# Optimization experiments

Measured on AMD Instinct MI355X. Metric: run time of the kernel, lower is better.

Reference implementation:

```python
import jax, jax.numpy as jnp
import numpy as np
from jax import lax

B, T, C = 2, 1024, 2048
H, N = 32, 64
LAYER_ID, N_LAYER = 1, 24
EPS = 1e-5 * 64.0  # 1e-5 * head_size_divisor**2, divisor=8
RESCALE_T = 256.0 * 0.7  # bf16_limit * 0.7


def setup_inputs():
    key = jax.random.key(0)
    ks = jax.random.split(key, 16)
    r01 = LAYER_ID / (N_LAYER - 1)
    r10 = 1.0 - LAYER_ID / N_LAYER
    ddd = np.arange(C, dtype=np.float64) / C
    pw = lambda p: jnp.asarray(1.0 - ddd ** p, jnp.float32)
    n = np.arange(C, dtype=np.float64)
    decay = -7.0 + 5.0 * (n / (C - 1)) ** (0.85 + r01 ** 0.5)
    sc = lambda k, shp, s: jax.random.normal(k, shp, jnp.float32) * s
    return {
        'x': sc(ks[0], (B, T, C), 1.0),
        'v_first': sc(ks[1], (B, T, C), 1.0),
        'x_r': pw(0.2 * r10), 'x_w': pw(0.9 * r10),
        'x_k': jnp.asarray(1.0 - (ddd ** (0.9 * r10) + 0.4 * r01), jnp.float32),
        'x_v': jnp.asarray(1.0 - (ddd ** (0.4 * r10) + 0.6 * r01), jnp.float32),
        'x_a': pw(0.9 * r10), 'x_g': pw(0.2 * r10),
        'w0': jnp.asarray(decay + 0.5, jnp.float32),
        'w1': sc(ks[2], (C, 64), 0.02), 'w2': sc(ks[3], (64, C), 0.02),
        'a0': jnp.zeros((C,), jnp.float32),
        'a1': sc(ks[4], (C, 64), 0.02), 'a2': sc(ks[5], (64, C), 0.02),
        'v0': jnp.ones((C,), jnp.float32),
        'v1': sc(ks[6], (C, 32), 0.02), 'v2': sc(ks[7], (32, C), 0.02),
        'g1': sc(ks[8], (C, 128), 0.02), 'g2': sc(ks[9], (128, C), 0.02),
        'k_k': jnp.full((C,), 0.85, jnp.float32),
        'k_a': jnp.ones((C,), jnp.float32),
        'r_k': sc(ks[10], (H, N), 0.05),
        'W_r': sc(ks[11], (C, C), C ** -0.5),
        'W_k': sc(ks[12], (C, C), C ** -0.5),
        'W_v': sc(ks[13], (C, C), C ** -0.5),
        'W_o': sc(ks[14], (C, C), C ** -0.5),
        'ln_w': jnp.ones((C,), jnp.float32),
        'ln_b': jnp.zeros((C,), jnp.float32),
    }


def wkv7(r, w, k, v, a, b):
    # RWKV-7 per-head linear state recurrence: S <- S*diag(w) + S a b^T + v k^T; out = S r
    Bsz, Tlen, Cd = r.shape
    to = lambda t: t.reshape(Bsz, Tlen, H, N).transpose(1, 0, 2, 3)  # (T,B,H,N)
    rr, kk, vv, aa, bb = map(to, (r, k, v, a, b))
    ww = jnp.exp(-jnp.exp(to(w)))  # decay in (0,1); w <= -0.5 guaranteed upstream

    def step(S, xs):
        rt, wt, kt, vt, at, bt = xs
        sa = jnp.einsum('bhij,bhj->bhi', S, at)
        S = S * wt[:, :, None, :] + sa[..., None] * bt[:, :, None, :] + vt[..., None] * kt[:, :, None, :]
        return S, jnp.einsum('bhij,bhj->bhi', S, rt)

    S0 = jnp.zeros((Bsz, H, N, N), r.dtype)
    _, out = lax.scan(step, S0, (rr, ww, kk, vv, aa, bb))
    return out.transpose(1, 0, 2, 3).reshape(Bsz, Tlen, Cd)


def reference(x, v_first, x_r, x_w, x_k, x_v, x_a, x_g, w0, w1, w2, a0, a1, a2,
              v0, v1, v2, g1, g2, k_k, k_a, r_k, W_r, W_k, W_v, W_o, ln_w, ln_b):
    # token shift (ZeroPad2d((0,0,1,-1)))
    xx = jnp.concatenate([jnp.zeros_like(x[:, :1]), x[:, :-1]], axis=1) - x
    xr = x + xx * x_r; xw = x + xx * x_w; xk = x + xx * x_k
    xv = x + xx * x_v; xa = x + xx * x_a; xg = x + xx * x_g
    r = xr @ W_r.T
    w = -jax.nn.softplus(-(w0 + jnp.tanh(xw @ w1) @ w2)) - 0.5  # soft clamp to (-inf,-0.5]
    k = xk @ W_k.T
    v = xv @ W_v.T
    # layer_id > 0: value residual gated toward v_first (with max-abs rescales)
    v1p = xv @ v1
    v1p = v1p / jnp.maximum(jnp.max(jnp.abs(v1p)), 1.0)
    v2p = v1p @ v2
    v2p = v2p / jnp.maximum(jnp.max(jnp.abs(v2p)), 1.0)
    gate = jax.nn.sigmoid(jnp.clip(v0 + v2p, -16.0, 16.0))
    vd = v_first - v
    vd = vd / jnp.maximum(jnp.max(jnp.abs(vd)), 1.0)
    v = v + vd * gate
    a = jax.nn.sigmoid(a0 + (xa @ a1) @ a2)
    g = jax.nn.sigmoid(xg @ g1) @ g2
    kk = (k * k_k).reshape(B, T, H, N)
    kk = (kk / jnp.maximum(jnp.linalg.norm(kk, axis=-1, keepdims=True), 1e-12)).reshape(B, T, C)
    k = k * (1.0 + (a - 1.0) * k_a)
    y = wkv7(r, w, k, v, -kk, kk * a)
    needs_rescale = jnp.max(jnp.abs(y)) > RESCALE_T
    # GroupNorm: H groups of size N
    yg = y.reshape(B, T, H, N)
    mu = yg.mean(-1, keepdims=True)
    var = yg.var(-1, keepdims=True)
    y = ((yg - mu) / jnp.sqrt(var + EPS)).reshape(B, T, C) * ln_w + ln_b
    y = y + ((r.reshape(B, T, H, N) * k.reshape(B, T, H, N) * r_k).sum(-1, keepdims=True)
             * v.reshape(B, T, H, N)).reshape(B, T, C)
    y = (y * g) @ W_o.T
    y = jnp.where(needs_rescale, y * 0.5, y)
    v_first_out = jnp.where(needs_rescale, v_first * 0.5, v_first)
    return y, v_first_out
```

## Files before the change

### kernel.cpp

```cpp
#include <hip/hip_runtime.h>
#include <hip/hip_bf16.h>

#define ELq 4194304
#define Cq 2048
#define Tq 1024
#define Hq 32
#define Mq 2048

typedef __attribute__((ext_vector_type(8))) short bf16x8;
typedef __attribute__((ext_vector_type(4))) float f32x4;

__device__ __forceinline__ unsigned short f2bu(float f) {
  union { float f; unsigned u; } v; v.f = f;
  unsigned r = v.u + 0x7fffu + ((v.u >> 16) & 1u);
  return (unsigned short)(r >> 16);
}
__device__ __forceinline__ float b2f(unsigned short u) {
  union { unsigned u; float f; } v; v.u = ((unsigned)u) << 16;
  return v.f;
}
__device__ __forceinline__ void gl_lds16(const void* g, void* l) {
  __builtin_amdgcn_global_load_lds((const __attribute__((address_space(1))) unsigned int*)g,
                                   (__attribute__((address_space(3))) unsigned int*)l, 16, 0, 0);
}

template<int CTRL>
__device__ __forceinline__ float dpp_add(float x) {
  int t = __builtin_amdgcn_update_dpp(0, __builtin_bit_cast(int, x), CTRL, 0xF, 0xF, true);
  return x + __builtin_bit_cast(float, t);
}

struct ConvJob { const float* src; unsigned short* dst; int rows, cols, trans; };
struct ConvJobs { ConvJob j[12]; };

__global__ void k_conv(ConvJobs jobs) {
  ConvJob jb = jobs.j[blockIdx.z];
  int n = jb.rows * jb.cols;
  if (!jb.trans) {
    int n4 = n >> 2;
    for (int i = blockIdx.x * blockDim.x + threadIdx.x; i < n4; i += gridDim.x * blockDim.x) {
      float4 v = ((const float4*)jb.src)[i];
      ushort4 o;
      o.x = f2bu(v.x); o.y = f2bu(v.y); o.z = f2bu(v.z); o.w = f2bu(v.w);
      ((ushort4*)jb.dst)[i] = o;
    }
  } else {
    for (int i = blockIdx.x * blockDim.x + threadIdx.x; i < n; i += gridDim.x * blockDim.x) {
      int col = i / jb.rows;
      int row = i - col * jb.rows;
      jb.dst[i] = f2bu(jb.src[(size_t)row * jb.cols + col]);
    }
  }
}

__global__ void k_zero(unsigned int* p) { if (threadIdx.x < 8) p[threadIdx.x] = 0u; }

__global__ void k_prologue(const float* __restrict__ x,
    const float* __restrict__ mr, const float* __restrict__ mw, const float* __restrict__ mk,
    const float* __restrict__ mv, const float* __restrict__ ma, const float* __restrict__ mg,
    unsigned short* __restrict__ xr, unsigned short* __restrict__ xw, unsigned short* __restrict__ xk,
    unsigned short* __restrict__ xv, unsigned short* __restrict__ xa, unsigned short* __restrict__ xg)
{
  int i4 = blockIdx.x * 256 + threadIdx.x;
  if (i4 >= ELq / 4) return;
  int i = i4 << 2;
  float4 xc = *(const float4*)(x + i);
  int t = (i >> 11) & (Tq - 1);
  float4 xp = make_float4(0.f, 0.f, 0.f, 0.f);
  if (t) xp = *(const float4*)(x + i - Cq);
  float4 dx = make_float4(xp.x - xc.x, xp.y - xc.y, xp.z - xc.z, xp.w - xc.w);
  int c = i & (Cq - 1);
  auto mix = [&](const float* __restrict__ m, unsigned short* __restrict__ o) {
    float4 mm = *(const float4*)(m + c);
    ushort4 u;
    u.x = f2bu(xc.x + dx.x * mm.x); u.y = f2bu(xc.y + dx.y * mm.y);
    u.z = f2bu(xc.z + dx.z * mm.z); u.w = f2bu(xc.w + dx.w * mm.w);
    *(ushort4*)(o + i) = u;
  };
  mix(mr, xr); mix(mw, xw); mix(mk, xk); mix(mv, xv); mix(ma, xa); mix(mg, xg);
}

struct GJob {
  const unsigned short* A; const unsigned short* B;
  const float* bias; float* Cf; unsigned short* Cb;
  unsigned int* amax; const float* aux;
  int K; int ld; int epi;
  float* kkp; float* abp; const float* kkw; const float* kaw;
};
struct GJobs { GJob j[4]; };

__device__ __forceinline__ void epi_store(int epi, float v, size_t o,
    float* Cf, unsigned short* Cb, const float* bias, const float* aux, int col, float& lmax)
{
  switch (epi) {
    case 0: Cf[o] = v; break;
    case 1: Cf[o] = v + bias[col]; break;
    case 2: Cf[o] = 1.f / (1.f + expf(-(v + bias[col]))); break;
    case 4: Cb[o] = f2bu(v); break;
    case 7: lmax = fmaxf(lmax, fabsf(v)); Cf[o] = v; break;
    case 9: lmax = fmaxf(lmax, fabsf(aux[o] - v)); Cf[o] = v; break;
    case 10: {
      float wv = v + bias[col];
      float wlog = -log1pf(expf(-wv)) - 0.5f;
      Cf[o] = expf(-expf(wlog));
      break;
    }
  }
}

__global__ __launch_bounds__(256, 2) void k_gemm128(GJobs jobs) {
  GJob jb = jobs.j[blockIdx.z];
  __shared__ __align__(16) unsigned short As[128 * 32];
  __shared__ __align__(16) unsigned short Bs[128 * 32];
  __shared__ float sred[4];
  const int tid = threadIdx.x, lane = tid & 63, wid = tid >> 6;
  const int wr = wid >> 1, wc = wid & 1;
  const int lin = blockIdx.y * 16 + blockIdx.x;
  const int swz = (lin & 7) * 32 + (lin >> 3);
  const int m0 = (swz >> 4) * 128, n0 = (swz & 15) * 128;
  const int K = jb.K, ld = jb.ld;
  const unsigned short* A = jb.A; const unsigned short* B = jb.B;
  f32x4 acc[4][4] = {};
  for (int k0 = 0; k0 < K; k0 += 32) {
    #pragma unroll
    for (int i = 0; i < 2; ++i) {
      int cw = wid * 64 + i * 256;
      int c = cw + lane;
      int row = c >> 2, q = c & 3;
      gl_lds16(A + (size_t)(m0 + row) * ld + k0 + q * 8, &As[cw * 8]);
      gl_lds16(B + (size_t)(n0 + row) * ld + k0 + q * 8, &Bs[cw * 8]);
    }
    __syncthreads();
    const int kg = (lane >> 4) * 8;
    bf16x8 af[4], bq[4];
    #pragma unroll
    for (int mi = 0; mi < 4; ++mi)
      af[mi] = *(const bf16x8*)&As[(wr * 64 + mi * 16 + (lane & 15)) * 32 + kg];
    #pragma unroll
    for (int ni = 0; ni < 4; ++ni)
      bq[ni] = *(const bf16x8*)&Bs[(wc * 64 + ni * 16 + (lane & 15)) * 32 + kg];
    #pragma unroll
    for (int mi = 0; mi < 4; ++mi)
      #pragma unroll
      for (int ni = 0; ni < 4; ++ni)
        acc[mi][ni] = __builtin_amdgcn_mfma_f32_16x16x32_bf16(af[mi], bq[ni], acc[mi][ni], 0, 0, 0);
    __syncthreads();
  }
  if (jb.epi == 11) {
    float kkwv[4], kawv[4]; int colv[4];
    #pragma unroll
    for (int ni = 0; ni < 4; ++ni) {
      colv[ni] = n0 + wc * 64 + ni * 16 + (lane & 15);
      kkwv[ni] = jb.kkw[colv[ni]];
      kawv[ni] = jb.kaw[colv[ni]];
    }
    #pragma unroll
    for (int mi = 0; mi < 4; ++mi) {
      #pragma unroll
      for (int q = 0; q < 4; ++q) {
        float kkv[4]; float ss = 0.f;
        #pragma unroll
        for (int ni = 0; ni < 4; ++ni) {
          kkv[ni] = acc[mi][ni][q] * kkwv[ni];
          ss += kkv[ni] * kkv[ni];
        }
        ss = dpp_add<0xB1>(ss); ss = dpp_add<0x4E>(ss);
        ss = dpp_add<0x141>(ss); ss = dpp_add<0x140>(ss);
        float inv = 1.f / fmaxf(sqrtf(ss), 1e-12f);
        int row = m0 + wr * 64 + mi * 16 + ((lane >> 4) << 2) + q;
        #pragma unroll
        for (int ni = 0; ni < 4; ++ni) {
          size_t o = (size_t)row * 2048 + colv[ni];
          float kraw = acc[mi][ni][q];
          float kkn = kkv[ni] * inv;
          float as = jb.abp[o];
          jb.kkp[o] = -kkn;
          jb.abp[o] = kkn * as;
          jb.Cf[o] = kraw * (1.f + (as - 1.f) * kawv[ni]);
        }
      }
    }
    return;
  }
  float lmax = 0.f;
  #pragma unroll
  for (int mi = 0; mi < 4; ++mi)
    #pragma unroll
    for (int ni = 0; ni < 4; ++ni) {
      int col = n0 + wc * 64 + ni * 16 + (lane & 15);
      int row = m0 + wr * 64 + mi * 16 + ((lane >> 4) << 2);
      #pragma unroll
      for (int q = 0; q < 4; ++q)
        epi_store(jb.epi, acc[mi][ni][q], (size_t)(row + q) * 2048 + col,
                  jb.Cf, jb.Cb, jb.bias, jb.aux, col, lmax);
    }
  if (jb.epi == 7 || jb.epi == 9) {
    #pragma unroll
    for (int o = 32; o; o >>= 1) lmax = fmaxf(lmax, __shfl_xor(lmax, o));
    if (lane == 0) sred[wid] = lmax;
    __syncthreads();
    if (tid == 0)
      atomicMax(jb.amax, __float_as_uint(fmaxf(fmaxf(sred[0], sred[1]), fmaxf(sred[2], sred[3]))));
  }
}

template<int TBN>
__global__ __launch_bounds__(256, 2) void k_gemmN_sk(GJob jb) {
  __shared__ __align__(16) unsigned short As[128 * 32];
  __shared__ __align__(16) unsigned short Bs[TBN * 32];
  const int tid = threadIdx.x, lane = tid & 63, wid = tid >> 6;
  const int m0 = blockIdx.x * 128;
  const int koff = blockIdx.y * 256;
  const int ld = jb.ld;
  constexpr int NF = TBN / 16;
  const unsigned short* A = jb.A + koff;
  const unsigned short* B = jb.B + koff;
  float* out = jb.Cf + (size_t)blockIdx.y * (2048 * TBN);
  f32x4 acc[2][NF] = {};
  for (int k0 = 0; k0 < 256; k0 += 32) {
    for (int cw = wid * 64; cw < 512; cw += 256) {
      int c = cw + lane; int row = c >> 2, q = c & 3;
      gl_lds16(A + (size_t)(m0 + row) * ld + k0 + q * 8, &As[cw * 8]);
    }
    for (int cw = wid * 64; cw < TBN * 4; cw += 256) {
      int c = cw + lane; int row = c >> 2, q = c & 3;
      gl_lds16(B + (size_t)row * ld + k0 + q * 8, &Bs[cw * 8]);
    }
    __syncthreads();
    const int kg = (lane >> 4) * 8;
    bf16x8 af[2], bq[NF];
    #pragma unroll
    for (int mi = 0; mi < 2; ++mi)
      af[mi] = *(const bf16x8*)&As[(wid * 32 + mi * 16 + (lane & 15)) * 32 + kg];
    #pragma unroll
    for (int ni = 0; ni < NF; ++ni)
      bq[ni] = *(const bf16x8*)&Bs[(ni * 16 + (lane & 15)) * 32 + kg];
    #pragma unroll
    for (int mi = 0; mi < 2; ++mi)
      #pragma unroll
      for (int ni = 0; ni < NF; ++ni)
        acc[mi][ni] = __builtin_amdgcn_mfma_f32_16x16x32_bf16(af[mi], bq[ni], acc[mi][ni], 0, 0, 0);
    __syncthreads();
  }
  #pragma unroll
  for (int mi = 0; mi < 2; ++mi)
    #pragma unroll
    for (int ni = 0; ni < NF; ++ni) {
      int col = ni * 16 + (lane & 15);
      int row = m0 + wid * 32 + mi * 16 + ((lane >> 4) << 2);
      #pragma unroll
      for (int q = 0; q < 4; ++q)
        out[(size_t)(row + q) * TBN + col] = acc[mi][ni][q];
    }
}

__global__ void k_skepi(const float* __restrict__ pw, const float* __restrict__ pa,
                        const float* __restrict__ pv, const float* __restrict__ pg,
                        unsigned short* __restrict__ hw, unsigned short* __restrict__ ha,
                        unsigned short* __restrict__ hv, unsigned short* __restrict__ hg,
                        unsigned int* __restrict__ amax) {
  int i = blockIdx.x * 256 + threadIdx.x;
  const float* src; unsigned short* dst; int stride, mode, loc;
  if (i < 131072)      { src = pw; dst = hw; stride = 131072; mode = 0; loc = i; }
  else if (i < 262144) { src = pa; dst = ha; stride = 131072; mode = 1; loc = i - 131072; }
  else if (i < 327680) { src = pv; dst = hv; stride = 65536;  mode = 2; loc = i - 262144; }
  else                 { src = pg; dst = hg; stride = 262144; mode = 3; loc = i - 327680; }
  float s = 0.f;
  #pragma unroll
  for (int sp = 0; sp < 8; ++sp) s += src[loc + (size_t)sp * stride];
  float lmax = 0.f, o;
  switch (mode) {
    case 0: o = tanhf(s); break;
    case 1: o = s; break;
    case 2: o = s; lmax = fabsf(s); break;
    default: o = 1.f / (1.f + expf(-s)); break;
  }
  dst[loc] = f2bu(o);
  #pragma unroll
  for (int of = 32; of; of >>= 1) lmax = fmaxf(lmax, __shfl_xor(lmax, of));
  if ((threadIdx.x & 63) == 0 && lmax > 0.f) atomicMax(amax, __float_as_uint(lmax));
}

__global__ void k_vfin(float* __restrict__ v, const float* __restrict__ vf,
                       const float* __restrict__ z, const float* __restrict__ v0c,
                       const unsigned int* __restrict__ sc) {
  int i4 = blockIdx.x * 256 + threadIdx.x;
  if (i4 >= ELq / 4) return;
  int i = i4 << 2;
  float m1 = fmaxf(__uint_as_float(sc[0]), 1.f);
  float m2 = fmaxf(__uint_as_float(sc[1]) / m1, 1.f);
  float inv12 = 1.f / (m1 * m2);
  float invvd = 1.f / fmaxf(__uint_as_float(sc[2]), 1.f);
  int c = i & (Cq - 1);
  float4 zv = *(const float4*)(z + i);
  float4 vv = *(const float4*)(v + i);
  float4 fv = *(const float4*)(vf + i);
  float4 v0v = *(const float4*)(v0c + c);
  float4 o;
  #pragma unroll
  for (int j = 0; j < 4; ++j) {
    float gx = (&v0v.x)[j] + (&zv.x)[j] * inv12;
    gx = fminf(fmaxf(gx, -16.f), 16.f);
    float gate = 1.f / (1.f + expf(-gx));
    float vr = (&vv.x)[j];
    (&o.x)[j] = vr + ((&fv.x)[j] - vr) * (gate * invvd);
  }
  *(float4*)(v + i) = o;
}

struct SRg { float4 r, w, k, a, b; float v; };

__device__ __forceinline__ void ld_g(SRg& R,
    const float* __restrict__ rS, const float* __restrict__ wS, const float* __restrict__ kS,
    const float* __restrict__ vS, const float* __restrict__ aS, const float* __restrict__ bS,
    size_t sb, int cl, int row) {
  R.r = *(const float4*)(rS + sb + cl);
  R.w = *(const float4*)(wS + sb + cl);
  R.k = *(const float4*)(kS + sb + cl);
  R.a = *(const float4*)(aS + sb + cl);
  R.b = *(const float4*)(bS + sb + cl);
  R.v = vS[sb + row];
}

__device__ __forceinline__ void wkv_step(const SRg& R, float S[4], float& ymx,
    float* __restrict__ y, size_t yoff, int lane) {
  float sa = (S[0]*R.a.x + S[1]*R.a.y) + (S[2]*R.a.z + S[3]*R.a.w);
  sa = dpp_add<0xB1>(sa);
  sa = dpp_add<0x4E>(sa);
  sa = dpp_add<0x141>(sa);
  sa = dpp_add<0x140>(sa);
  float vi = R.v;
  float s0 = S[0]*R.w.x + (sa*R.b.x + vi*R.k.x);
  float s1 = S[1]*R.w.y + (sa*R.b.y + vi*R.k.y);
  float s2 = S[2]*R.w.z + (sa*R.b.z + vi*R.k.z);
  float s3 = S[3]*R.w.w + (sa*R.b.w + vi*R.k.w);
  S[0]=s0; S[1]=s1; S[2]=s2; S[3]=s3;
  float yp = (s0*R.r.x + s1*R.r.y) + (s2*R.r.z + s3*R.r.w);
  yp = dpp_add<0xB1>(yp);
  yp = dpp_add<0x4E>(yp);
  yp = dpp_add<0x141>(yp);
  yp = dpp_add<0x140>(yp);
  if ((lane & 15) == 0) {
    y[yoff] = yp;
    ymx = fmaxf(ymx, fabsf(yp));
  }
}

__global__ __launch_bounds__(64, 1) void k_wkv(
    const float* __restrict__ rS, const float* __restrict__ wS, const float* __restrict__ kS,
    const float* __restrict__ vS, const float* __restrict__ aS, const float* __restrict__ bS,
    float* __restrict__ y, unsigned int* __restrict__ ymax) {
  const int lane = threadIdx.x;
  const int bh = blockIdx.x & 63;
  const int rq = blockIdx.x >> 6;
  const int row = rq * 4 + (lane >> 4);
  const int cl = (lane & 15) * 4;
  float S[4];
  #pragma unroll
  for (int q = 0; q < 4; ++q) S[q] = 0.f;
  const size_t base0 = (size_t)(bh >> 5) * Tq * Cq + (size_t)(bh & 31) * 64;

  SRg R0, R1, R2, R3;
  ld_g(R0, rS, wS, kS, vS, aS, bS, base0,          cl, row);
  ld_g(R1, rS, wS, kS, vS, aS, bS, base0 + Cq,     cl, row);
  ld_g(R2, rS, wS, kS, vS, aS, bS, base0 + 2 * Cq, cl, row);
  ld_g(R3, rS, wS, kS, vS, aS, bS, base0 + 3 * Cq, cl, row);

  float ymx = 0.f;
  for (int t = 0; t < Tq; t += 4) {
    int t4 = (t + 4 < Tq) ? t + 4 : Tq - 1;
    int t5 = (t + 5 < Tq) ? t + 5 : Tq - 1;
    int t6 = (t + 6 < Tq) ? t + 6 : Tq - 1;
    int t7 = (t + 7 < Tq) ? t + 7 : Tq - 1;
    wkv_step(R0, S, ymx, y, base0 + (size_t)t * Cq + row, lane);
    ld_g(R0, rS, wS, kS, vS, aS, bS, base0 + (size_t)t4 * Cq, cl, row);
    wkv_step(R1, S, ymx, y, base0 + (size_t)(t + 1) * Cq + row, lane);
    ld_g(R1, rS, wS, kS, vS, aS, bS, base0 + (size_t)t5 * Cq, cl, row);
    wkv_step(R2, S, ymx, y, base0 + (size_t)(t + 2) * Cq + row, lane);
    ld_g(R2, rS, wS, kS, vS, aS, bS, base0 + (size_t)t6 * Cq, cl, row);
    wkv_step(R3, S, ymx, y, base0 + (size_t)(t + 3) * Cq + row, lane);
    ld_g(R3, rS, wS, kS, vS, aS, bS, base0 + (size_t)t7 * Cq, cl, row);
  }
  #pragma unroll
  for (int o = 32; o; o >>= 1) ymx = fmaxf(ymx, __shfl_xor(ymx, o));
  if (lane == 0) atomicMax(ymax, __float_as_uint(ymx));
}

__global__ __launch_bounds__(256) void k_epi1(const float* __restrict__ y, const float* __restrict__ r,
    const float* __restrict__ k, const float* __restrict__ v, const unsigned short* __restrict__ g,
    const float* __restrict__ lnw, const float* __restrict__ lnb, const float* __restrict__ rk,
    unsigned short* __restrict__ yg) {
  int wid = threadIdx.x >> 6, lane = threadIdx.x & 63;
  int idx = blockIdx.x * 4 + wid;
  size_t off = (size_t)idx * 64 + lane;
  int c = ((idx & (Hq - 1)) << 6) | lane;
  float yv = y[off];
  float s = yv;
  #pragma unroll
  for (int o = 32; o; o >>= 1) s += __shfl_xor(s, o);
  float mu = s * (1.f / 64.f);
  float d = yv - mu;
  float vs = d * d;
  #pragma unroll
  for (int o = 32; o; o >>= 1) vs += __shfl_xor(vs, o);
  float yn = d / sqrtf(vs * (1.f / 64.f) + 6.4e-4f);
  float yo = yn * lnw[c] + lnb[c];
  float bon = r[off] * k[off] * rk[c];
  #pragma unroll
  for (int o = 32; o; o >>= 1) bon += __shfl_xor(bon, o);
  yo += bon * v[off];
  yg[off] = f2bu(yo * b2f(g[off]));
}

__global__ void k_wo_fin(const float* __restrict__ p0, const float* __restrict__ p1,
                         const unsigned int* __restrict__ sc, float* __restrict__ out) {
  int i = blockIdx.x * 256 + threadIdx.x;
  if (i >= ELq / 4) return;
  float s = (__uint_as_float(sc[3]) > 179.2f) ? 0.5f : 1.f;
  float4 a = ((const float4*)p0)[i];
  float4 b = ((const float4*)p1)[i];
  ((float4*)out)[i] = make_float4((a.x + b.x) * s, (a.y + b.y) * s,
                                  (a.z + b.z) * s, (a.w + b.w) * s);
}

__global__ void k_vout(const float* __restrict__ vf, const unsigned int* __restrict__ sc,
                       float* __restrict__ out) {
  int i = blockIdx.x * 256 + threadIdx.x;
  if (i >= ELq) return;
  float s = (__uint_as_float(sc[3]) > 179.2f) ? 0.5f : 1.f;
  out[i] = vf[i] * s;
}

extern "C" void kernel_launch(void* const* d_in, const int* in_sizes, int n_in,
                              void* d_out, int out_size, void* d_ws, size_t ws_size,
                              hipStream_t stream) {
  const float* x      = (const float*)d_in[0];
  const float* vfirst = (const float*)d_in[1];
  const float* x_r = (const float*)d_in[2];
  const float* x_w = (const float*)d_in[3];
  const float* x_k = (const float*)d_in[4];
  const float* x_v = (const float*)d_in[5];
  const float* x_a = (const float*)d_in[6];
  const float* x_g = (const float*)d_in[7];
  const float* w0 = (const float*)d_in[8];
  const float* w1 = (const float*)d_in[9];
  const float* w2 = (const float*)d_in[10];
  const float* a0 = (const float*)d_in[11];
  const float* a1 = (const float*)d_in[12];
  const float* a2 = (const float*)d_in[13];
  const float* v0 = (const float*)d_in[14];
  const float* v1 = (const float*)d_in[15];
  const float* v2 = (const float*)d_in[16];
  const float* g1 = (const float*)d_in[17];
  const float* g2 = (const float*)d_in[18];
  const float* k_k = (const float*)d_in[19];
  const float* k_a = (const float*)d_in[20];
  const float* r_k = (const float*)d_in[21];
  const float* W_r = (const float*)d_in[22];
  const float* W_k = (const float*)d_in[23];
  const float* W_v = (const float*)d_in[24];
  const float* W_o = (const float*)d_in[25];
  const float* lnw = (const float*)d_in[26];
  const float* lnb = (const float*)d_in[27];

  char* ws = (char*)d_ws;
  size_t off = 0;
  auto alloc = [&](size_t bytes) -> void* {
    void* p = ws + off; off += (bytes + 255) & ~(size_t)255; return p;
  };
  unsigned int* scal = (unsigned int*)alloc(256);
  float* kbuf  = (float*)alloc((size_t)ELq * 4);
  float* vbuf  = (float*)alloc((size_t)ELq * 4);
  float* wbuf  = (float*)alloc((size_t)ELq * 4);
  float* abuf  = (float*)alloc((size_t)ELq * 4);
  float* kkbuf = (float*)alloc((size_t)ELq * 4);
  float* ybuf  = (float*)alloc((size_t)ELq * 4);
  unsigned short* xrb = (unsigned short*)alloc((size_t)ELq * 2);
  unsigned short* xwb = (unsigned short*)alloc((size_t)ELq * 2);
  unsigned short* xkb = (unsigned short*)alloc((size_t)ELq * 2);
  unsigned short* xvb = (unsigned short*)alloc((size_t)ELq * 2);
  unsigned short* xab = (unsigned short*)alloc((size_t)ELq * 2);
  unsigned short* xgb = (unsigned short*)alloc((size_t)ELq * 2);
  unsigned short* gbuf = (unsigned short*)alloc((size_t)ELq * 2);
  unsigned short* ygb  = (unsigned short*)alloc((size_t)ELq * 2);
  unsigned short* WrB = (unsigned short*)alloc((size_t)ELq * 2);
  unsigned short* WkB = (unsigned short*)alloc((size_t)ELq * 2);
  unsigned short* WvB = (unsigned short*)alloc((size_t)ELq * 2);
  unsigned short* WoB = (unsigned short*)alloc((size_t)ELq * 2);
  unsigned short* w1T = (unsigned short*)alloc(64 * 2048 * 2);
  unsigned short* a1T = (unsigned short*)alloc(64 * 2048 * 2);
  unsigned short* v1T = (unsigned short*)alloc(32 * 2048 * 2);
  unsigned short* g1T = (unsigned short*)alloc(128 * 2048 * 2);
  unsigned short* w2T = (unsigned short*)alloc(2048 * 64 * 2);
  unsigned short* a2T = (unsigned short*)alloc(2048 * 64 * 2);
  unsigned short* v2T = (unsigned short*)alloc(2048 * 32 * 2);
  unsigned short* g2T = (unsigned short*)alloc(2048 * 128 * 2);
  unsigned short* hwb = (unsigned short*)alloc((size_t)Mq * 64 * 2);
  unsigned short* hab = (unsigned short*)alloc((size_t)Mq * 64 * 2);
  unsigned short* hvb = (unsigned short*)alloc((size_t)Mq * 32 * 2);
  unsigned short* hgb = (unsigned short*)alloc((size_t)Mq * 128 * 2);
  float* pskw = (float*)alloc((size_t)8 * Mq * 64 * 4);
  float* pska = (float*)alloc((size_t)8 * Mq * 64 * 4);
  float* pskv = (float*)alloc((size_t)8 * Mq * 32 * 4);
  float* pskg = (float*)alloc((size_t)8 * Mq * 128 * 4);
  float* rbuf = (float*)d_out;
  float* zbuf = (float*)d_out + ELq;
  float* yout = (float*)d_out;
  float* vfout = (float*)d_out + ELq;
  float* pWo0 = (float*)xrb;
  float* pWo1 = pWo0 + ELq;

  k_zero<<<1, 64, 0, stream>>>(scal);

  ConvJobs cj;
  cj.j[0]  = {W_r, WrB, Cq, Cq, 0};
  cj.j[1]  = {W_k, WkB, Cq, Cq, 0};
  cj.j[2]  = {W_v, WvB, Cq, Cq, 0};
  cj.j[3]  = {W_o, WoB, Cq, Cq, 0};
  cj.j[4]  = {w1, w1T, 2048, 64, 1};
  cj.j[5]  = {a1, a1T, 2048, 64, 1};
  cj.j[6]  = {v1, v1T, 2048, 32, 1};
  cj.j[7]  = {g1, g1T, 2048, 128, 1};
  cj.j[8]  = {w2, w2T, 64, 2048, 1};
  cj.j[9]  = {a2, a2T, 64, 2048, 1};
  cj.j[10] = {v2, v2T, 32, 2048, 1};
  cj.j[11] = {g2, g2T, 128, 2048, 1};
  k_conv<<<dim3(1024, 1, 12), 256, 0, stream>>>(cj);

  k_prologue<<<ELq / 1024, 256, 0, stream>>>(x, x_r, x_w, x_k, x_v, x_a, x_g,
                                             xrb, xwb, xkb, xvb, xab, xgb);

  GJob jw = {xwb, w1T, nullptr, pskw, nullptr, nullptr, nullptr, 256, 2048, 0};
  k_gemmN_sk<64><<<dim3(16, 8), 256, 0, stream>>>(jw);
  GJob ja = {xab, a1T, nullptr, pska, nullptr, nullptr, nullptr, 256, 2048, 0};
  k_gemmN_sk<64><<<dim3(16, 8), 256, 0, stream>>>(ja);
  GJob jv = {xvb, v1T, nullptr, pskv, nullptr, nullptr, nullptr, 256, 2048, 0};
  k_gemmN_sk<32><<<dim3(16, 8), 256, 0, stream>>>(jv);
  GJob jg = {xgb, g1T, nullptr, pskg, nullptr, nullptr, nullptr, 256, 2048, 0};
  k_gemmN_sk<128><<<dim3(16, 8), 256, 0, stream>>>(jg);
  k_skepi<<<2304, 256, 0, stream>>>(pskw, pska, pskv, pskg, hwb, hab, hvb, hgb, scal + 0);

  GJobs g3j;
  g3j.j[0] = {hwb, w2T, w0, wbuf, nullptr, nullptr, nullptr, 64, 64, 10};
  g3j.j[1] = {hab, a2T, a0, abuf, nullptr, nullptr, nullptr, 64, 64, 2};
  g3j.j[2] = {hvb, v2T, nullptr, zbuf, nullptr, scal + 1, nullptr, 32, 32, 7};
  g3j.j[3] = {hgb, g2T, nullptr, nullptr, gbuf, nullptr, nullptr, 128, 128, 4};
  k_gemm128<<<dim3(16, 16, 4), 256, 0, stream>>>(g3j);

  GJobs g1j;
  g1j.j[0] = {xrb, WrB, nullptr, rbuf, nullptr, nullptr, nullptr, 2048, 2048, 0};
  g1j.j[1] = {xkb, WkB, nullptr, kbuf, nullptr, nullptr, nullptr, 2048, 2048, 11,
              kkbuf, abuf, k_k, k_a};
  g1j.j[2] = {xvb, WvB, nullptr, vbuf, nullptr, scal + 2, vfirst, 2048, 2048, 9};
  g1j.j[3] = g1j.j[0];
  k_gemm128<<<dim3(16, 16, 3), 256, 0, stream>>>(g1j);

  k_vfin<<<ELq / 1024, 256, 0, stream>>>(vbuf, vfirst, zbuf, v0, scal);
  k_wkv<<<16 * 2 * Hq, 64, 0, stream>>>(rbuf, wbuf, kbuf, vbuf, kkbuf, abuf, ybuf, scal + 3);
  k_epi1<<<(2 * Tq * Hq) / 4, 256, 0, stream>>>(ybuf, rbuf, kbuf, vbuf, gbuf, lnw, lnb, r_k, ygb);

  GJobs gfj;
  gfj.j[0] = {ygb, WoB, nullptr, pWo0, nullptr, nullptr, nullptr, 1024, 2048, 0};
  gfj.j[1] = {ygb + 1024, WoB + 1024, nullptr, pWo1, nullptr, nullptr, nullptr, 1024, 2048, 0};
  gfj.j[2] = gfj.j[0]; gfj.j[3] = gfj.j[0];
  k_gemm128<<<dim3(16, 16, 2), 256, 0, stream>>>(gfj);
  k_wo_fin<<<ELq / 1024, 256, 0, stream>>>(pWo0, pWo1, scal, yout);

  k_vout<<<ELq / 256, 256, 0, stream>>>(vfirst, scal, vfout);
}
```

Baseline: 551.3 us.

## Merge small launches and deepen WKV prefetch to eight timesteps

Zeroing the scalar buffer moves into the conversion kernel, and the four skinny LoRA GEMMs become one launch dispatched by blockIdx.z. The output-scale and v_first-scale kernels merge into one vectorized kernel. The WKV recurrence now prefetches eight timesteps ahead instead of four, to hide more global-load latency. The aim is fewer launches and better latency hiding in the serial scan, at the cost of more registers per WKV lane and shared-memory sizing for the largest skinny tile in every block.

```diff
diff --git a/kernel.cpp b/kernel.cpp
--- a/kernel.cpp
+++ b/kernel.cpp
@@ -31,9 +31,10 @@
 }
 
 struct ConvJob { const float* src; unsigned short* dst; int rows, cols, trans; };
-struct ConvJobs { ConvJob j[12]; };
+struct ConvJobs { ConvJob j[12]; unsigned int* scal; };
 
 __global__ void k_conv(ConvJobs jobs) {
+  if (blockIdx.z == 0 && blockIdx.x == 0 && threadIdx.x < 8) jobs.scal[threadIdx.x] = 0u;
   ConvJob jb = jobs.j[blockIdx.z];
   int n = jb.rows * jb.cols;
   if (!jb.trans) {
@@ -52,8 +53,6 @@
     }
   }
 }
-
-__global__ void k_zero(unsigned int* p) { if (threadIdx.x < 8) p[threadIdx.x] = 0u; }
 
 __global__ void k_prologue(const float* __restrict__ x,
     const float* __restrict__ mr, const float* __restrict__ mw, const float* __restrict__ mk,
@@ -205,9 +204,8 @@
 }
 
 template<int TBN>
-__global__ __launch_bounds__(256, 2) void k_gemmN_sk(GJob jb) {
-  __shared__ __align__(16) unsigned short As[128 * 32];
-  __shared__ __align__(16) unsigned short Bs[TBN * 32];
+__device__ __forceinline__ void sk_body(const GJob& jb,
+    unsigned short* __restrict__ As, unsigned short* __restrict__ Bs) {
   const int tid = threadIdx.x, lane = tid & 63, wid = tid >> 6;
   const int m0 = blockIdx.x * 128;
   const int koff = blockIdx.y * 256;
@@ -252,6 +250,17 @@
       for (int q = 0; q < 4; ++q)
         out[(size_t)(row + q) * TBN + col] = acc[mi][ni][q];
     }
+}
+
+__global__ __launch_bounds__(256, 2) void k_skinny(GJobs jobs) {
+  __shared__ __align__(16) unsigned short As[128 * 32];
+  __shared__ __align__(16) unsigned short Bs[128 * 32];
+  switch (blockIdx.z) {
+    case 0:  sk_body<64>(jobs.j[0], As, Bs); break;
+    case 1:  sk_body<64>(jobs.j[1], As, Bs); break;
+    case 2:  sk_body<32>(jobs.j[2], As, Bs); break;
+    default: sk_body<128>(jobs.j[3], As, Bs); break;
+  }
 }
 
 __global__ void k_skepi(const float* __restrict__ pw, const float* __restrict__ pa,
@@ -360,26 +369,42 @@
   for (int q = 0; q < 4; ++q) S[q] = 0.f;
   const size_t base0 = (size_t)(bh >> 5) * Tq * Cq + (size_t)(bh & 31) * 64;
 
-  SRg R0, R1, R2, R3;
+  SRg R0, R1, R2, R3, R4, R5, R6, R7;
   ld_g(R0, rS, wS, kS, vS, aS, bS, base0,          cl, row);
   ld_g(R1, rS, wS, kS, vS, aS, bS, base0 + Cq,     cl, row);
   ld_g(R2, rS, wS, kS, vS, aS, bS, base0 + 2 * Cq, cl, row);
   ld_g(R3, rS, wS, kS, vS, aS, bS, base0 + 3 * Cq, cl, row);
+  ld_g(R4, rS, wS, kS, vS, aS, bS, base0 + 4 * Cq, cl, row);
+  ld_g(R5, rS, wS, kS, vS, aS, bS, base0 + 5 * Cq, cl, row);
+  ld_g(R6, rS, wS, kS, vS, aS, bS, base0 + 6 * Cq, cl, row);
+  ld_g(R7, rS, wS, kS, vS, aS, bS, base0 + 7 * Cq, cl, row);
 
   float ymx = 0.f;
-  for (int t = 0; t < Tq; t += 4) {
-    int t4 = (t + 4 < Tq) ? t + 4 : Tq - 1;
-    int t5 = (t + 5 < Tq) ? t + 5 : Tq - 1;
-    int t6 = (t + 6 < Tq) ? t + 6 : Tq - 1;
-    int t7 = (t + 7 < Tq) ? t + 7 : Tq - 1;
+  for (int t = 0; t < Tq; t += 8) {
+    int n0 = (t + 8  < Tq) ? t + 8  : Tq - 1;
+    int n1 = (t + 9  < Tq) ? t + 9  : Tq - 1;
+    int n2 = (t + 10 < Tq) ? t + 10 : Tq - 1;
+    int n3 = (t + 11 < Tq) ? t + 11 : Tq - 1;
+    int n4 = (t + 12 < Tq) ? t + 12 : Tq - 1;
+    int n5 = (t + 13 < Tq) ? t + 13 : Tq - 1;
+    int n6 = (t + 14 < Tq) ? t + 14 : Tq - 1;
+    int n7 = (t + 15 < Tq) ? t + 15 : Tq - 1;
     wkv_step(R0, S, ymx, y, base0 + (size_t)t * Cq + row, lane);
-    ld_g(R0, rS, wS, kS, vS, aS, bS, base0 + (size_t)t4 * Cq, cl, row);
+    ld_g(R0, rS, wS, kS, vS, aS, bS, base0 + (size_t)n0 * Cq, cl, row);
     wkv_step(R1, S, ymx, y, base0 + (size_t)(t + 1) * Cq + row, lane);
-    ld_g(R1, rS, wS, kS, vS, aS, bS, base0 + (size_t)t5 * Cq, cl, row);
+    ld_g(R1, rS, wS, kS, vS, aS, bS, base0 + (size_t)n1 * Cq, cl, row);
     wkv_step(R2, S, ymx, y, base0 + (size_t)(t + 2) * Cq + row, lane);
-    ld_g(R2, rS, wS, kS, vS, aS, bS, base0 + (size_t)t6 * Cq, cl, row);
+    ld_g(R2, rS, wS, kS, vS, aS, bS, base0 + (size_t)n2 * Cq, cl, row);
     wkv_step(R3, S, ymx, y, base0 + (size_t)(t + 3) * Cq + row, lane);
-    ld_g(R3, rS, wS, kS, vS, aS, bS, base0 + (size_t)t7 * Cq, cl, row);
+    ld_g(R3, rS, wS, kS, vS, aS, bS, base0 + (size_t)n3 * Cq, cl, row);
+    wkv_step(R4, S, ymx, y, base0 + (size_t)(t + 4) * Cq + row, lane);
+    ld_g(R4, rS, wS, kS, vS, aS, bS, base0 + (size_t)n4 * Cq, cl, row);
+    wkv_step(R5, S, ymx, y, base0 + (size_t)(t + 5) * Cq + row, lane);
+    ld_g(R5, rS, wS, kS, vS, aS, bS, base0 + (size_t)n5 * Cq, cl, row);
+    wkv_step(R6, S, ymx, y, base0 + (size_t)(t + 6) * Cq + row, lane);
+    ld_g(R6, rS, wS, kS, vS, aS, bS, base0 + (size_t)n6 * Cq, cl, row);
+    wkv_step(R7, S, ymx, y, base0 + (size_t)(t + 7) * Cq + row, lane);
+    ld_g(R7, rS, wS, kS, vS, aS, bS, base0 + (size_t)n7 * Cq, cl, row);
   }
   #pragma unroll
   for (int o = 32; o; o >>= 1) ymx = fmaxf(ymx, __shfl_xor(ymx, o));
@@ -412,23 +437,21 @@
   yg[off] = f2bu(yo * b2f(g[off]));
 }
 
-__global__ void k_wo_fin(const float* __restrict__ p0, const float* __restrict__ p1,
-                         const unsigned int* __restrict__ sc, float* __restrict__ out) {
+__global__ void k_fin(const float* __restrict__ p0, const float* __restrict__ p1,
+                      const unsigned int* __restrict__ sc, float* __restrict__ yout,
+                      const float* __restrict__ vf, float* __restrict__ vfout) {
   int i = blockIdx.x * 256 + threadIdx.x;
-  if (i >= ELq / 4) return;
   float s = (__uint_as_float(sc[3]) > 179.2f) ? 0.5f : 1.f;
-  float4 a = ((const float4*)p0)[i];
-  float4 b = ((const float4*)p1)[i];
-  ((float4*)out)[i] = make_float4((a.x + b.x) * s, (a.y + b.y) * s,
-                                  (a.z + b.z) * s, (a.w + b.w) * s);
-}
-
-__global__ void k_vout(const float* __restrict__ vf, const unsigned int* __restrict__ sc,
-                       float* __restrict__ out) {
-  int i = blockIdx.x * 256 + threadIdx.x;
-  if (i >= ELq) return;
-  float s = (__uint_as_float(sc[3]) > 179.2f) ? 0.5f : 1.f;
-  out[i] = vf[i] * s;
+  if (i < ELq / 4) {
+    float4 a = ((const float4*)p0)[i];
+    float4 b = ((const float4*)p1)[i];
+    ((float4*)yout)[i] = make_float4((a.x + b.x) * s, (a.y + b.y) * s,
+                                     (a.z + b.z) * s, (a.w + b.w) * s);
+  } else {
+    int j = i - ELq / 4;
+    float4 vv = ((const float4*)vf)[j];
+    ((float4*)vfout)[j] = make_float4(vv.x * s, vv.y * s, vv.z * s, vv.w * s);
+  }
 }
 
 extern "C" void kernel_launch(void* const* d_in, const int* in_sizes, int n_in,
@@ -510,8 +533,6 @@
   float* pWo0 = (float*)xrb;
   float* pWo1 = pWo0 + ELq;
 
-  k_zero<<<1, 64, 0, stream>>>(scal);
-
   ConvJobs cj;
   cj.j[0]  = {W_r, WrB, Cq, Cq, 0};
   cj.j[1]  = {W_k, WkB, Cq, Cq, 0};
@@ -525,19 +546,18 @@
   cj.j[9]  = {a2, a2T, 64, 2048, 1};
   cj.j[10] = {v2, v2T, 32, 2048, 1};
   cj.j[11] = {g2, g2T, 128, 2048, 1};
+  cj.scal = scal;
   k_conv<<<dim3(1024, 1, 12), 256, 0, stream>>>(cj);
 
   k_prologue<<<ELq / 1024, 256, 0, stream>>>(x, x_r, x_w, x_k, x_v, x_a, x_g,
                                              xrb, xwb, xkb, xvb, xab, xgb);
 
-  GJob jw = {xwb, w1T, nullptr, pskw, nullptr, nullptr, nullptr, 256, 2048, 0};
-  k_gemmN_sk<64><<<dim3(16, 8), 256, 0, stream>>>(jw);
-  GJob ja = {xab, a1T, nullptr, pska, nullptr, nullptr, nullptr, 256, 2048, 0};
-  k_gemmN_sk<64><<<dim3(16, 8), 256, 0, stream>>>(ja);
-  GJob jv = {xvb, v1T, nullptr, pskv, nullptr, nullptr, nullptr, 256, 2048, 0};
-  k_gemmN_sk<32><<<dim3(16, 8), 256, 0, stream>>>(jv);
-  GJob jg = {xgb, g1T, nullptr, pskg, nullptr, nullptr, nullptr, 256, 2048, 0};
-  k_gemmN_sk<128><<<dim3(16, 8), 256, 0, stream>>>(jg);
+  GJobs gsk;
+  gsk.j[0] = {xwb, w1T, nullptr, pskw, nullptr, nullptr, nullptr, 256, 2048, 0};
+  gsk.j[1] = {xab, a1T, nullptr, pska, nullptr, nullptr, nullptr, 256, 2048, 0};
+  gsk.j[2] = {xvb, v1T, nullptr, pskv, nullptr, nullptr, nullptr, 256, 2048, 0};
+  gsk.j[3] = {xgb, g1T, nullptr, pskg, nullptr, nullptr, nullptr, 256, 2048, 0};
+  k_skinny<<<dim3(16, 8, 4), 256, 0, stream>>>(gsk);
   k_skepi<<<2304, 256, 0, stream>>>(pskw, pska, pskv, pskg, hwb, hab, hvb, hgb, scal + 0);
 
   GJobs g3j;
@@ -564,7 +584,5 @@
   gfj.j[1] = {ygb + 1024, WoB + 1024, nullptr, pWo1, nullptr, nullptr, nullptr, 1024, 2048, 0};
   gfj.j[2] = gfj.j[0]; gfj.j[3] = gfj.j[0];
   k_gemm128<<<dim3(16, 16, 2), 256, 0, stream>>>(gfj);
-  k_wo_fin<<<ELq / 1024, 256, 0, stream>>>(pWo0, pWo1, scal, yout);
-
-  k_vout<<<ELq / 256, 256, 0, stream>>>(vfirst, scal, vfout);
-}
+  k_fin<<<ELq / 512, 256, 0, stream>>>(pWo0, pWo1, scal, yout, vfirst, vfout);
+}
```

Result: faster. 510.3 us (-7.4%).
